# Kernel tuning notes

Hardware: AMD Instinct MI355X
Metric: run time of the kernel (lower is better)

Reference implementation:

```python
import jax, jax.numpy as jnp
import numpy as np
from jax import lax

EPS = 1e-5

def setup_inputs() -> dict:
    key = jax.random.key(0)
    k1, k2, k3, k4, k5, k6 = jax.random.split(key, 6)
    x = jax.random.normal(k1, (1, 64, 31, 96, 96), dtype=jnp.float32)
    # small init scale keeps gate pre-activations in a sane range
    w = jax.random.normal(k2, (256, 64, 3, 3, 3), dtype=jnp.float32) * 0.05
    gamma = jax.random.uniform(k3, (256,), dtype=jnp.float32)
    beta = jax.random.normal(k4, (256,), dtype=jnp.float32) * 0.1
    mean = jax.random.normal(k5, (256,), dtype=jnp.float32) * 0.1
    var = jax.random.uniform(k6, (256,), dtype=jnp.float32) + 0.5
    return {"x": x, "w": w, "gamma": gamma, "beta": beta, "mean": mean, "var": var}

def _bcast(p):
    return p[None, :, None, None, None]

def reference(x, w, gamma, beta, mean, var):
    # Conv3d (bias=False), stride 1, padding 1, NCDHW
    gates = lax.conv_general_dilated(
        x, w, window_strides=(1, 1, 1), padding=[(1, 1)] * 3,
        dimension_numbers=("NCDHW", "OIDHW", "NCDHW"))
    # BatchNorm3d (inference, running stats)
    scale = gamma * lax.rsqrt(var + EPS)
    gates = gates * _bcast(scale) + _bcast(beta - mean * scale)
    C = 64  # out_channels
    Wx = jnp.tanh(gates[:, 0 * C:1 * C])
    ft = jax.nn.sigmoid(gates[:, 1 * C:2 * C])
    rt = jax.nn.sigmoid(gates[:, 2 * C:3 * C])
    X = jnp.tanh(gates[:, 3 * C:4 * C])  # act == 'tanh'
    # time axis (dim 2) to front: (D, B, C, H, W)
    Wt = jnp.moveaxis(Wx, 2, 0)
    Ft = jnp.moveaxis(ft, 2, 0)
    Rt = jnp.moveaxis(rt, 2, 0)
    Xt = jnp.moveaxis(X, 2, 0)
    # t = 0: Ct = 1 - ft (note: Wx unused at first step, per source)
    C0 = 1.0 - Ft[0]
    h0 = Rt[0] * C0 + (1.0 - Rt[0]) * Xt[0]
    def step(Ct, inp):
        wx, f, r, xx = inp
        Ct = f * Ct + (1.0 - f) * wx
        ht = r * Ct + (1.0 - r) * xx
        return Ct, ht
    _, hs = lax.scan(step, C0, (Wt[1:], Ft[1:], Rt[1:], Xt[1:]))
    hts = jnp.concatenate([h0[None], hs], axis=0)  # (D,B,C,H,W)
    return jnp.moveaxis(hts, 0, 2)  # (B,C,D,H,W)
```

## Files before the change

### kernel.cpp

```cpp
#include <hip/hip_runtime.h>
#include <cstddef>

#define CI_  64
#define CO_  256
#define DD_  31
#define HH_  96
#define WW_  96
#define HW_  (HH_*WW_)
#define DHW_ (DD_*HW_)
#define EPSV 1e-5f

#define PD_   33
#define PH_   98
#define PW_   98
#define PHW_  9604
#define PDHW_ 316932

#define S_COL 8
#define S_CIG 144
#define S_ROW 1152
#define S_DD  11520
#define NTASK 4320
#define NTASKP 4352
#define XH_N  (NTASKP*8)

#define NTILE 72
#define NBLK  (NTILE*DD_)
#define GSP   128

#define PREP_RB 216
#define PREP_PB 1239
#define PREP_TB 279
#define PREP_NB (PREP_RB + PREP_PB + PREP_TB)

typedef _Float16 half8   __attribute__((ext_vector_type(8)));
typedef _Float16 half4v  __attribute__((ext_vector_type(4)));
typedef float    float4v __attribute__((ext_vector_type(4)));

__device__ __forceinline__ void gl_lds16(const _Float16* g, _Float16* l) {
  __builtin_amdgcn_global_load_lds(
      (const __attribute__((address_space(1))) unsigned int*)(g),
      (__attribute__((address_space(3))) unsigned int*)(l), 16, 0, 0);
}

__global__ __launch_bounds__(256) void prep_k(const float* __restrict__ w,
                                              const float* __restrict__ x,
                                              _Float16* __restrict__ wr2,
                                              _Float16* __restrict__ xt) {
  const int bid = blockIdx.x;
  if (bid < PREP_RB) {
    int idx = bid * 256 + threadIdx.x;
    int lw   = idx & 15;
    int quad = (idx >> 4) & 3;
    int cog  = (idx >> 6) & 15;
    int tkc  = idx >> 10;
    int kc   = tkc & 1;
    int t    = tkc >> 1;
    int co   = cog * 16 + lw;
    int cib  = kc * 32 + quad * 8;
    half8 v;
#pragma unroll
    for (int s = 0; s < 8; s++)
      v[s] = (_Float16)w[(size_t)co * 1728 + (size_t)(cib + s) * 27 + t];
    *(half8*)(wr2 + (size_t)idx * 8) = v;
  } else if (bid < PREP_RB + PREP_PB) {
    int p = (bid - PREP_RB) * 256 + threadIdx.x;
    if (p >= PDHW_) return;
    int pd  = p / PHW_;
    int rem = p - pd * PHW_;
    int ph  = rem / PW_;
    int pw  = rem - ph * PW_;
    bool in = (pd >= 1) & (pd <= DD_) & (ph >= 1) & (ph <= HH_) & (pw >= 1) & (pw <= WW_);
    if (in) return;
    half8 z = (half8)(_Float16)0.f;
#pragma unroll
    for (int cig = 0; cig < 8; cig++)
      *(half8*)(xt + ((size_t)cig * PDHW_ + p) * 8) = z;
  } else {
    int idx = (bid - PREP_RB - PREP_PB) * 256 + threadIdx.x;
    if (idx >= 31 * 96 * 24) return;
    int wq  = idx % 24;
    int rem = idx / 24;
    int h   = rem % 96;
    int d   = rem / 96;
    const float* xp = x + (size_t)d * HW_ + (size_t)h * WW_ + wq * 4;
    size_t p0 = (size_t)(d + 1) * PHW_ + (size_t)(h + 1) * PW_ + (wq * 4 + 1);
#pragma unroll 1
    for (int cig = 0; cig < 8; cig++) {
      float4 vv[8];
#pragma unroll
      for (int s = 0; s < 8; s++)
        vv[s] = *(const float4*)(xp + (size_t)(cig * 8 + s) * DHW_);
#pragma unroll
      for (int k = 0; k < 4; k++) {
        half8 o;
#pragma unroll
        for (int s = 0; s < 8; s++) o[s] = (_Float16)(&vv[s].x)[k];
        *(half8*)(xt + ((size_t)cig * PDHW_ + p0 + k) * 8) = o;
      }
    }
  }
}

__device__ __forceinline__ float tanh_f(float v) {
  float t = __expf(-2.f * fabsf(v));
  return copysignf((1.f - t) * __builtin_amdgcn_rcpf(1.f + t), v);
}
__device__ __forceinline__ float sigm_f(float v) {
  return __builtin_amdgcn_rcpf(1.f + __expf(-v));
}

__global__ __launch_bounds__(512, 4) void conv_mfma_k(
    const _Float16* __restrict__ xt, const _Float16* __restrict__ wr2,
    const float* __restrict__ gamma, const float* __restrict__ beta,
    const float* __restrict__ mean, const float* __restrict__ var,
    _Float16* __restrict__ gates)
{
  __shared__ _Float16 xh[XH_N];

  const int bid  = blockIdx.x;
  const int flat = (bid & 7) * 279 + (bid >> 3);
  const int d    = flat / NTILE;
  const int bx   = flat - d * NTILE;
  const int wti  = bx % 6;
  const int hti  = bx / 6;
  const int h0   = hti * 8, w0 = wti * 16;

  const int tid  = threadIdx.x;
  const int lane = tid & 63;
  const int wave = __builtin_amdgcn_readfirstlane(tid >> 6);
  const int wm   = wave >> 2;
  const int wn   = wave & 3;
  const int lw   = lane & 15;
  const int quad = lane >> 4;

#pragma unroll 1
  for (int it = 0; it < 9; ++it) {
    const int wb = it * 512 + wave * 64;
    if (wb < NTASKP) {
      const int task = wb + lane;
      const int tt   = task < NTASK ? task : (NTASK - 1);
      int col = tt % 18;
      int rc  = tt / 18;
      int cig = rc & 7;
      int dr  = rc >> 3;
      int dd  = dr / 10;
      int row = dr - dd * 10;
      const _Float16* g = xt + (((size_t)cig * PDHW_ + (size_t)(d + dd) * PHW_ +
                                 (size_t)(h0 + row) * PW_ + (w0 + col)) << 3);
      gl_lds16(g, xh + (size_t)wb * 8);
    }
  }

  float4v acc[4][4];
#pragma unroll
  for (int m = 0; m < 4; m++)
#pragma unroll
    for (int j = 0; j < 4; j++) acc[m][j] = (float4v)0.f;

  __syncthreads();

  const int abase0 = quad * S_CIG + lw * S_COL + (wm * 4) * S_ROW;

#define LOADB(bf, s)                                                          \
  {                                                                           \
    const int t9_ = (s) / 6, sub_ = (s) - 6 * t9_;                            \
    const int kc_ = sub_ / 3, kw_ = sub_ - 3 * kc_;                           \
    const int t_  = t9_ * 3 + kw_;                                            \
    const _Float16* bp_ =                                                     \
        wr2 + (((size_t)((t_ * 2 + kc_) * 16 + wn * 4)) << 9) + (lane << 3);  \
    bf[0] = *(const half8*)(bp_);                                             \
    bf[1] = *(const half8*)(bp_ + (1 << 9));                                  \
    bf[2] = *(const half8*)(bp_ + (2 << 9));                                  \
    bf[3] = *(const half8*)(bp_ + (3 << 9));                                  \
  }

#define STEP(s, bf)                                                           \
  {                                                                           \
    const int t9_ = (s) / 6, sub_ = (s) - 6 * t9_;                            \
    const int kc_ = sub_ / 3, kw_ = sub_ - 3 * kc_;                           \
    const int kd_ = t9_ / 3, kh_ = t9_ - 3 * kd_;                             \
    const int ab_ = abase0 + kd_ * S_DD + kh_ * S_ROW + kc_ * (4 * S_CIG) +   \
                    kw_ * S_COL;                                              \
    half8 af0 = *(const half8*)(xh + ab_);                                    \
    half8 af1 = *(const half8*)(xh + ab_ + S_ROW);                            \
    half8 af2 = *(const half8*)(xh + ab_ + 2 * S_ROW);                        \
    half8 af3 = *(const half8*)(xh + ab_ + 3 * S_ROW);                        \
    __builtin_amdgcn_s_setprio(1);                                            \
    _Pragma("unroll")                                                         \
    for (int j = 0; j < 4; ++j) {                                             \
      acc[0][j] = __builtin_amdgcn_mfma_f32_16x16x32_f16(af0, bf[j], acc[0][j], 0, 0, 0); \
      acc[1][j] = __builtin_amdgcn_mfma_f32_16x16x32_f16(af1, bf[j], acc[1][j], 0, 0, 0); \
      acc[2][j] = __builtin_amdgcn_mfma_f32_16x16x32_f16(af2, bf[j], acc[2][j], 0, 0, 0); \
      acc[3][j] = __builtin_amdgcn_mfma_f32_16x16x32_f16(af3, bf[j], acc[3][j], 0, 0, 0); \
    }                                                                         \
    __builtin_amdgcn_s_setprio(0);                                            \
  }

  half8 bfa[4], bfb[4];
  LOADB(bfa, 0)
#pragma unroll 1
  for (int i = 0; i < 27; ++i) {
    const int s0 = 2 * i;
    LOADB(bfb, s0 + 1)
    STEP(s0, bfa)
    if (i < 26) LOADB(bfa, s0 + 2)
    STEP(s0 + 1, bfb)
  }
#undef LOADB
#undef STEP

  __syncthreads();

  _Float16* wt = xh + wave * 4096;
  const bool istanh = (wn == 0) || (wn == 3);
#pragma unroll
  for (int j = 0; j < 4; j++) {
    const int co  = wn * 64 + j * 16 + lw;
    const int col = j * 16 + lw;
    const float s  = gamma[co] * rsqrtf(var[co] + EPSV);
    const float bb = fmaf(-mean[co], s, beta[co]);
    const int key = (col & 7) << 3;
#pragma unroll
    for (int m = 0; m < 4; m++) {
      half4v hv;
#pragma unroll
      for (int reg = 0; reg < 4; reg++) {
        float v = fmaf(acc[m][j][reg], s, bb);
        float a;
        if (istanh) a = tanh_f(v); else a = sigm_f(v);
        hv[reg] = (_Float16)a;
      }
      *(half4v*)(wt + col * 64 + ((m * 16 + quad * 4) ^ key)) = hv;
    }
  }
  _Float16* gb = gates + ((size_t)(d * NTILE + bx) * 256 + wn * 64) * GSP + wm * 64;
  const int rb = (lane & 7) * 8;
#pragma unroll
  for (int s8 = 0; s8 < 8; s8++) {
    const int col = s8 * 8 + (lane >> 3);
    half8 rv = *(const half8*)(wt + col * 64 + (rb ^ ((col & 7) << 3)));
    *(half8*)(gb + (size_t)col * GSP + rb) = rv;
  }
}

__global__ __launch_bounds__(256) void recurrence_k(const _Float16* __restrict__ gates,
                                                    float* __restrict__ out) {
  const int idx = blockIdx.x * 256 + threadIdx.x;
  const int q   = idx & 31;
  const int t2  = idx >> 5;
  const int c   = t2 / NTILE;
  const int bx  = t2 - c * NTILE;
  const int hti = bx / 6, wti = bx - hti * 6;
  const int sp  = q * 4;
  const int h   = hti * 8 + (sp >> 4);
  const int w   = wti * 16 + (sp & 15);

  const size_t DSTR = (size_t)NTILE * 256 * GSP;
  const _Float16* g0 = gates + (size_t)bx * 256 * GSP + sp;
  float* op = out + (size_t)c * DHW_ + (size_t)h * WW_ + w;

#define LD(dv, gate) (*(const half4v*)(g0 + (size_t)(dv) * DSTR + (size_t)(c + ((gate) << 6)) * GSP))

  half4v cf = LD(0, 1), cr = LD(0, 2), cx = LD(0, 3);
  half4v nwx = LD(1, 0), nf = LD(1, 1), nr = LD(1, 2), nx = LD(1, 3);
  float C[4];
  {
    float4 st;
#pragma unroll
    for (int k = 0; k < 4; k++) {
      C[k] = 1.f - (float)cf[k];
      float r0 = (float)cr[k], x0 = (float)cx[k];
      (&st.x)[k] = fmaf(r0, C[k] - x0, x0);
    }
    *(float4*)op = st;
  }
#pragma unroll 1
  for (int d = 1; d < DD_; d++) {
    half4v cwx = nwx; cf = nf; cr = nr; cx = nx;
    if (d < DD_ - 1) {
      nwx = LD(d + 1, 0); nf = LD(d + 1, 1);
      nr  = LD(d + 1, 2); nx = LD(d + 1, 3);
    }
    float4 st;
#pragma unroll
    for (int k = 0; k < 4; k++) {
      float wx0 = (float)cwx[k], f0 = (float)cf[k], r0 = (float)cr[k], x0 = (float)cx[k];
      C[k] = fmaf(f0, C[k] - wx0, wx0);
      (&st.x)[k] = fmaf(r0, C[k] - x0, x0);
    }
    *(float4*)(op + (size_t)d * HW_) = st;
  }
#undef LD
}

extern "C" void kernel_launch(void* const* d_in, const int* in_sizes, int n_in,
                              void* d_out, int out_size, void* d_ws, size_t ws_size,
                              hipStream_t stream) {
  const float* x     = (const float*)d_in[0];
  const float* w     = (const float*)d_in[1];
  const float* gamma = (const float*)d_in[2];
  const float* beta  = (const float*)d_in[3];
  const float* mean  = (const float*)d_in[4];
  const float* var   = (const float*)d_in[5];
  float* out = (float*)d_out;

  _Float16* wr2   = (_Float16*)d_ws;
  _Float16* xt    = (_Float16*)((char*)d_ws + 884736);
  _Float16* gates = (_Float16*)((char*)d_ws + 884736 + 40567296);

  prep_k<<<PREP_NB, 256, 0, stream>>>(w, x, wr2, xt);
  conv_mfma_k<<<NBLK, 512, 0, stream>>>(xt, wr2, gamma, beta, mean, var, gates);
  recurrence_k<<<(64 * NTILE * 32) / 256, 256, 0, stream>>>(gates, out);
}
```

Before: 422.8 us.

## Interleave four gates per spatial quad in gate buffer and drop LDS transpose

The conv epilogue now writes each 4-pixel group of all four gates contiguously (16 halves) straight from registers into a new gate layout, removing the LDS staging, the __syncthreads and the swizzled transposed copy-out. The recurrence kernel then reads each timestep with two 16-byte loads instead of four 8-byte loads from separate gate planes. The main MFMA loop is also fully unrolled. The direct global stores from the epilogue are 8-byte scattered writes, which may coalesce worse than the previous staged 16-byte writes, and full unrolling increases code size and register pressure.

Result: no change. 422.6 us (-0.1%).

```diff
diff --git a/kernel.cpp b/kernel.cpp
--- a/kernel.cpp
+++ b/kernel.cpp
@@ -26,7 +26,9 @@
 
 #define NTILE 72
 #define NBLK  (NTILE*DD_)
-#define GSP   128
+
+#define GBLK 32768
+#define GDSTR ((size_t)NTILE * GBLK)
 
 #define PREP_RB 216
 #define PREP_PB 1239
@@ -199,7 +201,7 @@
 
   half8 bfa[4], bfb[4];
   LOADB(bfa, 0)
-#pragma unroll 1
+#pragma unroll
   for (int i = 0; i < 27; ++i) {
     const int s0 = 2 * i;
     LOADB(bfb, s0 + 1)
@@ -210,37 +212,25 @@
 #undef LOADB
 #undef STEP
 
-  __syncthreads();
-
-  _Float16* wt = xh + wave * 4096;
+  _Float16* gb = gates + (size_t)(d * NTILE + bx) * GBLK + wn * 4;
   const bool istanh = (wn == 0) || (wn == 3);
 #pragma unroll
   for (int j = 0; j < 4; j++) {
-    const int co  = wn * 64 + j * 16 + lw;
-    const int col = j * 16 + lw;
+    const int co = wn * 64 + j * 16 + lw;
+    const int c  = j * 16 + lw;
     const float s  = gamma[co] * rsqrtf(var[co] + EPSV);
     const float bb = fmaf(-mean[co], s, beta[co]);
-    const int key = (col & 7) << 3;
 #pragma unroll
     for (int m = 0; m < 4; m++) {
       half4v hv;
 #pragma unroll
       for (int reg = 0; reg < 4; reg++) {
         float v = fmaf(acc[m][j][reg], s, bb);
-        float a;
-        if (istanh) a = tanh_f(v); else a = sigm_f(v);
-        hv[reg] = (_Float16)a;
+        hv[reg] = (_Float16)(istanh ? tanh_f(v) : sigm_f(v));
       }
-      *(half4v*)(wt + col * 64 + ((m * 16 + quad * 4) ^ key)) = hv;
-    }
-  }
-  _Float16* gb = gates + ((size_t)(d * NTILE + bx) * 256 + wn * 64) * GSP + wm * 64;
-  const int rb = (lane & 7) * 8;
-#pragma unroll
-  for (int s8 = 0; s8 < 8; s8++) {
-    const int col = s8 * 8 + (lane >> 3);
-    half8 rv = *(const half8*)(wt + col * 64 + (rb ^ ((col & 7) << 3)));
-    *(half8*)(gb + (size_t)col * GSP + rb) = rv;
+      const int q = (wm * 4 + m) * 4 + quad;
+      *(half4v*)(gb + (size_t)c * 512 + q * 16) = hv;
+    }
   }
 }
 
@@ -256,42 +246,43 @@
   const int h   = hti * 8 + (sp >> 4);
   const int w   = wti * 16 + (sp & 15);
 
-  const size_t DSTR = (size_t)NTILE * 256 * GSP;
-  const _Float16* g0 = gates + (size_t)bx * 256 * GSP + sp;
+  const _Float16* g0 = gates + (size_t)bx * GBLK + (size_t)c * 512 + q * 16;
   float* op = out + (size_t)c * DHW_ + (size_t)h * WW_ + w;
 
-#define LD(dv, gate) (*(const half4v*)(g0 + (size_t)(dv) * DSTR + (size_t)(c + ((gate) << 6)) * GSP))
-
-  half4v cf = LD(0, 1), cr = LD(0, 2), cx = LD(0, 3);
-  half4v nwx = LD(1, 0), nf = LD(1, 1), nr = LD(1, 2), nx = LD(1, 3);
+#define LDLO(dv) (*(const half8*)(g0 + (size_t)(dv) * GDSTR))
+#define LDHI(dv) (*(const half8*)(g0 + (size_t)(dv) * GDSTR + 8))
+
+  half8 clo = LDLO(0), chi = LDHI(0);
+  half8 nlo = LDLO(1), nhi = LDHI(1);
   float C[4];
   {
     float4 st;
 #pragma unroll
     for (int k = 0; k < 4; k++) {
-      C[k] = 1.f - (float)cf[k];
-      float r0 = (float)cr[k], x0 = (float)cx[k];
+      C[k] = 1.f - (float)clo[4 + k];
+      float r0 = (float)chi[k], x0 = (float)chi[4 + k];
       (&st.x)[k] = fmaf(r0, C[k] - x0, x0);
     }
     *(float4*)op = st;
   }
 #pragma unroll 1
   for (int d = 1; d < DD_; d++) {
-    half4v cwx = nwx; cf = nf; cr = nr; cx = nx;
+    clo = nlo; chi = nhi;
     if (d < DD_ - 1) {
-      nwx = LD(d + 1, 0); nf = LD(d + 1, 1);
-      nr  = LD(d + 1, 2); nx = LD(d + 1, 3);
+      nlo = LDLO(d + 1); nhi = LDHI(d + 1);
     }
     float4 st;
 #pragma unroll
     for (int k = 0; k < 4; k++) {
-      float wx0 = (float)cwx[k], f0 = (float)cf[k], r0 = (float)cr[k], x0 = (float)cx[k];
+      float wx0 = (float)clo[k],     f0 = (float)clo[4 + k];
+      float r0  = (float)chi[k],     x0 = (float)chi[4 + k];
       C[k] = fmaf(f0, C[k] - wx0, wx0);
       (&st.x)[k] = fmaf(r0, C[k] - x0, x0);
     }
     *(float4*)(op + (size_t)d * HW_) = st;
   }
-#undef LD
+#undef LDLO
+#undef LDHI
 }
 
 extern "C" void kernel_launch(void* const* d_in, const int* in_sizes, int n_in,
```
